# Kernel optimization log

Hardware: AMD Instinct MI355X
Metric: run time of the kernel (lower is better)

The kernel has to match this reference:

```python
import jax, jax.numpy as jnp
import numpy as np

B, T, C, H = 2, 2048, 1024, 16
D = C // H  # head_dim = 64


def setup_inputs() -> dict:
    key = jax.random.key(0)
    ks = jax.random.split(key, 12)
    s = 1.0 / np.sqrt(C)
    inp = {
        "q": jax.random.normal(ks[0], (B, T, C), jnp.float32),
        "k": jax.random.normal(ks[1], (B, T, C), jnp.float32),
        "v": jax.random.normal(ks[2], (B, T, C), jnp.float32),
        "mask": jnp.tril(jnp.ones((T, T), jnp.int32)),  # causal mask; 0 = masked
        "Wq": jax.random.normal(ks[3], (C, C), jnp.float32) * s,
        "bq": jax.random.normal(ks[4], (C,), jnp.float32) * s,
        "Wk": jax.random.normal(ks[5], (C, C), jnp.float32) * s,
        "bk": jax.random.normal(ks[6], (C,), jnp.float32) * s,
        "Wv": jax.random.normal(ks[7], (C, C), jnp.float32) * s,
        "bv": jax.random.normal(ks[8], (C,), jnp.float32) * s,
        "Wo": jax.random.normal(ks[9], (C, C), jnp.float32) * s,
        "bo": jax.random.normal(ks[10], (C,), jnp.float32) * s,
    }
    return inp


def reference(q, k, v, mask, Wq, bq, Wk, bk, Wv, bv, Wo, bo):
    # Linear projections (torch Linear: x @ W.T + b)
    qh = (q @ Wq.T + bq).reshape(B, T, H, D).transpose(0, 2, 1, 3)  # [B,H,T,D]
    kh = (k @ Wk.T + bk).reshape(B, -1, H, D).transpose(0, 2, 1, 3)
    vh = (v @ Wv.T + bv).reshape(B, -1, H, D).transpose(0, 2, 1, 3)
    scores = jnp.einsum("bhtd,bhsd->bhts", qh, kh) / jnp.sqrt(jnp.float32(D))
    scores = jnp.where(mask[None, None, :, :] == 0, -jnp.inf, scores)
    attn = jax.nn.softmax(scores, axis=-1)
    out = jnp.einsum("bhts,bhsd->bhtd", attn, vh)  # [B,H,T,D]
    out = out.transpose(0, 2, 1, 3).reshape(B, T, C)
    return out @ Wo.T + bo
```

## Files before the change

### kernel.cpp

```cpp
#include <hip/hip_runtime.h>
#include <hip/hip_bf16.h>

#define BB 2
#define TT 2048
#define CC 1024
#define HH 16
#define DD 64
#define MM (BB * TT)

typedef __bf16 bf16;
typedef __bf16 bf16x4 __attribute__((ext_vector_type(4)));
typedef __bf16 bf16x8 __attribute__((ext_vector_type(8)));
typedef float f32x4 __attribute__((ext_vector_type(4)));

__device__ __forceinline__ void gload16(const bf16* g, bf16* l) {
    __builtin_amdgcn_global_load_lds(
        (__attribute__((address_space(1))) void*)g,
        (__attribute__((address_space(3))) void*)l, 16, 0, 0);
}

__global__ __launch_bounds__(256) void to_bf16(
    const float* __restrict__ q, const float* __restrict__ k,
    const float* __restrict__ v,
    const float* __restrict__ wq, const float* __restrict__ wk,
    const float* __restrict__ wv, const float* __restrict__ wo,
    bf16* __restrict__ xq, bf16* __restrict__ xk, bf16* __restrict__ xv,
    bf16* __restrict__ owq, bf16* __restrict__ owk, bf16* __restrict__ owv,
    bf16* __restrict__ owo)
{
    const unsigned XE = 1u << 22;
    const unsigned WE = 1u << 20;
    const unsigned NC = (3u * XE + 4u * WE) >> 3;
    for (unsigned c = blockIdx.x * blockDim.x + threadIdx.x; c < NC;
         c += gridDim.x * blockDim.x) {
        const unsigned e = c << 3;
        const float* src; bf16* dst; unsigned off;
        if (e < 3u * XE) {
            const unsigned t = e >> 22; off = e & (XE - 1u);
            src = (t == 0) ? q : (t == 1) ? k : v;
            dst = (t == 0) ? xq : (t == 1) ? xk : xv;
        } else {
            const unsigned e2 = e - 3u * XE;
            const unsigned t = e2 >> 20; off = e2 & (WE - 1u);
            src = (t == 0) ? wq : (t == 1) ? wk : (t == 2) ? wv : wo;
            dst = (t == 0) ? owq : (t == 1) ? owk : (t == 2) ? owv : owo;
        }
        const f32x4 a = *reinterpret_cast<const f32x4*>(src + off);
        const f32x4 b = *reinterpret_cast<const f32x4*>(src + off + 4);
        bf16x8 r;
#pragma unroll
        for (int j = 0; j < 4; ++j) { r[j] = (bf16)a[j]; r[j + 4] = (bf16)b[j]; }
        *reinterpret_cast<bf16x8*>(dst + off) = r;
    }
}

template <typename TOUT, int HEAD_LAYOUT>
__device__ __forceinline__ void gemm_tile_body(
    const bf16* __restrict__ X, const bf16* __restrict__ W,
    const float* __restrict__ bias, TOUT* __restrict__ out,
    bf16* lA, bf16* lB, int vmode)
{
    const int tid  = threadIdx.x;
    const int lane = tid & 63;
    const int quad = lane >> 4;
    const int lm   = lane & 15;
    const int wave = tid >> 6;
    const int m0 = blockIdx.x << 7;
    const int n0 = blockIdx.y << 7;
    const int wrow = (wave >> 1) << 6;
    const int wcol = (wave & 1) << 6;

    const int c0 = tid, c1 = tid + 256;
    const bf16* gA0 = X + (size_t)(m0 + (c0 >> 2)) * CC + (c0 & 3) * 8;
    const bf16* gA1 = X + (size_t)(m0 + (c1 >> 2)) * CC + (c1 & 3) * 8;
    const bf16* gB0 = W + (size_t)(n0 + (c0 >> 2)) * CC + (c0 & 3) * 8;
    const bf16* gB1 = W + (size_t)(n0 + (c1 >> 2)) * CC + (c1 & 3) * 8;
    bf16* lAw0 = lA + wave * 512;
    bf16* lAw1 = lA + 2048 + wave * 512;
    bf16* lBw0 = lB + wave * 512;
    bf16* lBw1 = lB + 2048 + wave * 512;

    f32x4 acc[4][4];
#pragma unroll
    for (int i = 0; i < 4; ++i)
#pragma unroll
        for (int j = 0; j < 4; ++j) acc[i][j] = (f32x4){0.f, 0.f, 0.f, 0.f};

    for (int kk = 0; kk < CC; kk += 32) {
        __syncthreads();
        gload16(gA0 + kk, lAw0);
        gload16(gA1 + kk, lAw1);
        gload16(gB0 + kk, lBw0);
        gload16(gB1 + kk, lBw1);
        __syncthreads();

        bf16x8 af[4], bf_[4];
#pragma unroll
        for (int i = 0; i < 4; ++i)
            af[i] = *reinterpret_cast<const bf16x8*>(
                lA + (wrow + i * 16 + lm) * 32 + quad * 8);
#pragma unroll
        for (int j = 0; j < 4; ++j)
            bf_[j] = *reinterpret_cast<const bf16x8*>(
                lB + (wcol + j * 16 + lm) * 32 + quad * 8);
#pragma unroll
        for (int i = 0; i < 4; ++i)
#pragma unroll
            for (int j = 0; j < 4; ++j)
                acc[i][j] = __builtin_amdgcn_mfma_f32_16x16x32_bf16(
                    af[i], bf_[j], acc[i][j], 0, 0, 0);
    }

#pragma unroll
    for (int j = 0; j < 4; ++j) {
        const int col = n0 + wcol + j * 16 + lm;
        const float bv = bias[col];
        if (vmode) {
            const int h = col / DD, d = col % DD;
#pragma unroll
            for (int i = 0; i < 4; ++i) {
                const int m = m0 + wrow + i * 16 + quad * 4;
                const int b_ = m / TT, t = m % TT;
                bf16x4 o;
#pragma unroll
                for (int r = 0; r < 4; ++r) o[r] = (bf16)(acc[i][j][r] + bv);
                *reinterpret_cast<bf16x4*>(
                    (bf16*)out + (((size_t)(b_ * HH + h)) * DD + d) * TT + t) = o;
            }
        } else {
#pragma unroll
            for (int i = 0; i < 4; ++i)
#pragma unroll
                for (int r = 0; r < 4; ++r) {
                    const int m = m0 + wrow + i * 16 + quad * 4 + r;
                    const float v = acc[i][j][r] + bv;
                    if (HEAD_LAYOUT) {
                        const int b_ = m / TT, t = m % TT;
                        const int h = col / DD, d = col % DD;
                        out[(((size_t)(b_ * HH + h)) * TT + t) * DD + d] = (TOUT)v;
                    } else {
                        out[(size_t)m * CC + col] = (TOUT)v;
                    }
                }
        }
    }
}

__global__ __launch_bounds__(256) void gemm_qkv(
    const bf16* __restrict__ x0, const bf16* __restrict__ x1,
    const bf16* __restrict__ x2,
    const bf16* __restrict__ w0, const bf16* __restrict__ w1,
    const bf16* __restrict__ w2,
    const float* __restrict__ b0, const float* __restrict__ b1,
    const float* __restrict__ b2,
    bf16* __restrict__ o0, bf16* __restrict__ o1, bf16* __restrict__ o2)
{
    __shared__ __align__(16) bf16 lA[128 * 32];
    __shared__ __align__(16) bf16 lB[128 * 32];
    const int z = blockIdx.z;
    const bf16* X = (z == 0) ? x0 : (z == 1) ? x1 : x2;
    const bf16* W = (z == 0) ? w0 : (z == 1) ? w1 : w2;
    const float* bias = (z == 0) ? b0 : (z == 1) ? b1 : b2;
    bf16* out = (z == 0) ? o0 : (z == 1) ? o1 : o2;
    gemm_tile_body<bf16, 1>(X, W, bias, out, lA, lB, (z == 2) ? 1 : 0);
}

__global__ __launch_bounds__(256) void gemm_oproj(
    const bf16* __restrict__ X, const bf16* __restrict__ W,
    const float* __restrict__ bias, float* __restrict__ out)
{
    __shared__ __align__(16) bf16 lA[128 * 32];
    __shared__ __align__(16) bf16 lB[128 * 32];
    gemm_tile_body<float, 0>(X, W, bias, out, lA, lB, 0);
}

__global__ __launch_bounds__(256) void attn_fused(
    const bf16* __restrict__ Qh, const bf16* __restrict__ Kh,
    const bf16* __restrict__ Vt, bf16* __restrict__ attn_out)
{
    __shared__ __align__(16) bf16 ldsK[64 * 72];
    __shared__ __align__(16) bf16 ldsV[16 * 64 * 4];

    const int tid  = threadIdx.x;
    const int lane = tid & 63;
    const int wave = tid >> 6;
    const int xp = blockIdx.x;
    const int bh = blockIdx.y;
    const int b_ = bh >> 4, h = bh & 15;
    const size_t baseQK = (size_t)bh * TT * DD;
    const size_t baseVT = (size_t)bh * DD * TT;
    const int lm   = lane & 15;
    const int quad = lane >> 4;
    const int koff = quad * 8;

    const int kKey = tid >> 3, kDc = tid & 7;
    const int vD   = tid >> 2, vSc = tid & 3;

    for (int pass = 0; pass < 2; ++pass) {
        const int qb = pass == 0 ? (TT / 64 - 1 - xp) : xp;
        const int q0 = qb * 64 + wave * 16;
        const int q_lane = q0 + lm;

        const bf16* qp = Qh + baseQK + (size_t)q_lane * DD + koff;
        bf16x8 qr0 = *reinterpret_cast<const bf16x8*>(qp);
        bf16x8 qr1 = *reinterpret_cast<const bf16x8*>(qp + 32);
        bf16x8 qf0, qf1;
#pragma unroll
        for (int j = 0; j < 8; ++j) {
            qf0[j] = (bf16)((float)qr0[j] * 0.125f);
            qf1[j] = (bf16)((float)qr1[j] * 0.125f);
        }

        f32x4 Oacc[4];
#pragma unroll
        for (int dt = 0; dt < 4; ++dt) Oacc[dt] = (f32x4){0.f, 0.f, 0.f, 0.f};
        float m_run = -1e30f, l_run = 0.f;

        for (int kb = 0; kb <= qb; ++kb) {
            const int s0 = kb * 64;

            __syncthreads();
#pragma unroll
            for (int it = 0; it < 2; ++it) {
                const int key = kKey + it * 32;
                bf16x8 kv = *reinterpret_cast<const bf16x8*>(
                    Kh + baseQK + (size_t)(s0 + key) * DD + kDc * 8);
                *reinterpret_cast<bf16x8*>(&ldsK[key * 72 + kDc * 8]) = kv;
            }
#pragma unroll
            for (int it = 0; it < 2; ++it) {
                const int sc = vSc + it * 4;
                bf16x8 vv = *reinterpret_cast<const bf16x8*>(
                    Vt + baseVT + (size_t)vD * TT + s0 + sc * 8);
                bf16x4 lo, hi;
#pragma unroll
                for (int j = 0; j < 4; ++j) { lo[j] = vv[j]; hi[j] = vv[4 + j]; }
                *reinterpret_cast<bf16x4*>(&ldsV[((2 * sc) * 64 + vD) * 4]) = lo;
                *reinterpret_cast<bf16x4*>(&ldsV[((2 * sc + 1) * 64 + vD) * 4]) = hi;
            }
            __syncthreads();

            float sv[4][4];
#pragma unroll
            for (int st = 0; st < 4; ++st) {
                const bf16* kp = &ldsK[(st * 16 + lm) * 72 + koff];
                bf16x8 k0 = *reinterpret_cast<const bf16x8*>(kp);
                bf16x8 k1 = *reinterpret_cast<const bf16x8*>(kp + 32);
                f32x4 s = {0.f, 0.f, 0.f, 0.f};
                s = __builtin_amdgcn_mfma_f32_16x16x32_bf16(k0, qf0, s, 0, 0, 0);
                s = __builtin_amdgcn_mfma_f32_16x16x32_bf16(k1, qf1, s, 0, 0, 0);
#pragma unroll
                for (int r = 0; r < 4; ++r) sv[st][r] = s[r];
            }
            if (kb == qb) {
#pragma unroll
                for (int st = 0; st < 4; ++st) {
                    const int kbase = s0 + st * 16 + quad * 4;
#pragma unroll
                    for (int r = 0; r < 4; ++r)
                        if (kbase + r > q_lane) sv[st][r] = -1e30f;
                }
            }

            float mx = sv[0][0];
#pragma unroll
            for (int st = 0; st < 4; ++st)
#pragma unroll
                for (int r = 0; r < 4; ++r) mx = fmaxf(mx, sv[st][r]);
            mx = fmaxf(mx, __shfl_xor(mx, 16));
            mx = fmaxf(mx, __shfl_xor(mx, 32));
            if (__any(mx > m_run)) {
                const float mn = fmaxf(m_run, mx);
                const float alpha = __expf(m_run - mn);
                m_run = mn;
                l_run *= alpha;
#pragma unroll
                for (int dt = 0; dt < 4; ++dt) Oacc[dt] *= alpha;
            }
            float srow = 0.f;
#pragma unroll
            for (int st = 0; st < 4; ++st)
#pragma unroll
                for (int r = 0; r < 4; ++r) {
                    const float p = __expf(sv[st][r] - m_run);
                    sv[st][r] = p;
                    srow += p;
                }
            srow += __shfl_xor(srow, 16);
            srow += __shfl_xor(srow, 32);
            l_run += srow;

            bf16x8 pf[2];
#pragma unroll
            for (int c = 0; c < 2; ++c)
#pragma unroll
                for (int j = 0; j < 4; ++j) {
                    pf[c][j]     = (bf16)sv[2 * c][j];
                    pf[c][4 + j] = (bf16)sv[2 * c + 1][j];
                }

#pragma unroll
            for (int dt = 0; dt < 4; ++dt) {
                const int d = dt * 16 + lm;
#pragma unroll
                for (int c = 0; c < 2; ++c) {
                    bf16x4 v0 = *reinterpret_cast<const bf16x4*>(
                        &ldsV[((c * 8 + quad) * 64 + d) * 4]);
                    bf16x4 v1 = *reinterpret_cast<const bf16x4*>(
                        &ldsV[((c * 8 + 4 + quad) * 64 + d) * 4]);
                    bf16x8 vf;
#pragma unroll
                    for (int j = 0; j < 4; ++j) { vf[j] = v0[j]; vf[4 + j] = v1[j]; }
                    Oacc[dt] = __builtin_amdgcn_mfma_f32_16x16x32_bf16(
                        vf, pf[c], Oacc[dt], 0, 0, 0);
                }
            }
        }

        const float inv_l = 1.0f / l_run;
        bf16* dst = attn_out + ((size_t)(b_ * TT + q_lane)) * CC + h * DD;
#pragma unroll
        for (int dt = 0; dt < 4; ++dt) {
            bf16x4 o;
#pragma unroll
            for (int r = 0; r < 4; ++r) o[r] = (bf16)(Oacc[dt][r] * inv_l);
            *reinterpret_cast<bf16x4*>(dst + dt * 16 + quad * 4) = o;
        }
    }
}

extern "C" void kernel_launch(void* const* d_in, const int* in_sizes, int n_in,
                              void* d_out, int out_size, void* d_ws,
                              size_t ws_size, hipStream_t stream)
{
    const float* q  = (const float*)d_in[0];
    const float* k  = (const float*)d_in[1];
    const float* v  = (const float*)d_in[2];
    const float* Wq = (const float*)d_in[4];
    const float* bq = (const float*)d_in[5];
    const float* Wk = (const float*)d_in[6];
    const float* bk = (const float*)d_in[7];
    const float* Wv = (const float*)d_in[8];
    const float* bv = (const float*)d_in[9];
    const float* Wo = (const float*)d_in[10];
    const float* bo = (const float*)d_in[11];
    float* out = (float*)d_out;

    bf16* Qh   = (bf16*)d_ws;
    bf16* Kh   = Qh + (size_t)MM * CC;
    bf16* Vt   = Kh + (size_t)MM * CC;
    bf16* attn = Vt + (size_t)MM * CC;
    bf16* Xq   = attn + (size_t)MM * CC;
    bf16* Xk   = Xq + (size_t)MM * CC;
    bf16* Xv   = Xk + (size_t)MM * CC;
    bf16* Wqb  = Xv + (size_t)MM * CC;
    bf16* Wkb  = Wqb + (size_t)CC * CC;
    bf16* Wvb  = Wkb + (size_t)CC * CC;
    bf16* Wob  = Wvb + (size_t)CC * CC;

    const dim3 blk(256);
    to_bf16<<<dim3(2048), blk, 0, stream>>>(
        q, k, v, Wq, Wk, Wv, Wo, Xq, Xk, Xv, Wqb, Wkb, Wvb, Wob);
    gemm_qkv<<<dim3(MM / 128, CC / 128, 3), blk, 0, stream>>>(
        Xq, Xk, Xv, Wqb, Wkb, Wvb, bq, bk, bv, Qh, Kh, Vt);
    attn_fused<<<dim3(TT / 128, BB * HH), blk, 0, stream>>>(Qh, Kh, Vt, attn);
    gemm_oproj<<<dim3(MM / 128, CC / 128), blk, 0, stream>>>(
        attn, Wob, bo, out);
}
```

Before: 240.3 us.

## Double-buffer K/V tiles in attention with register prefetch and MFMA priority

The attention kernel now keeps two LDS buffers for the K and V tiles. It prefetches the next key block's K/V into registers while the current block is being computed, which removes one barrier per iteration and overlaps global-load latency with MFMA work. It also wraps the MFMA sections in s_setprio to favour matrix issue. The cost is doubled LDS use and extra registers, which may lower occupancy.

After: 234.7 us. 2.3% less time.

```diff
diff --git a/kernel.cpp b/kernel.cpp
--- a/kernel.cpp
+++ b/kernel.cpp
@@ -178,8 +178,8 @@
     const bf16* __restrict__ Qh, const bf16* __restrict__ Kh,
     const bf16* __restrict__ Vt, bf16* __restrict__ attn_out)
 {
-    __shared__ __align__(16) bf16 ldsK[64 * 72];
-    __shared__ __align__(16) bf16 ldsV[16 * 64 * 4];
+    __shared__ __align__(16) bf16 ldsK[2][64 * 72];
+    __shared__ __align__(16) bf16 ldsV[2][16 * 64 * 4];
 
     const int tid  = threadIdx.x;
     const int lane = tid & 63;
@@ -216,34 +216,55 @@
         for (int dt = 0; dt < 4; ++dt) Oacc[dt] = (f32x4){0.f, 0.f, 0.f, 0.f};
         float m_run = -1e30f, l_run = 0.f;
 
+        bf16x8 kreg[2], vreg[2];
+#pragma unroll
+        for (int it = 0; it < 2; ++it) {
+            kreg[it] = *reinterpret_cast<const bf16x8*>(
+                Kh + baseQK + (size_t)(kKey + it * 32) * DD + kDc * 8);
+            vreg[it] = *reinterpret_cast<const bf16x8*>(
+                Vt + baseVT + (size_t)vD * TT + (vSc + it * 4) * 8);
+        }
+        __syncthreads();
+
         for (int kb = 0; kb <= qb; ++kb) {
-            const int s0 = kb * 64;
-
-            __syncthreads();
+            const int cur = kb & 1;
+
 #pragma unroll
             for (int it = 0; it < 2; ++it) {
                 const int key = kKey + it * 32;
-                bf16x8 kv = *reinterpret_cast<const bf16x8*>(
-                    Kh + baseQK + (size_t)(s0 + key) * DD + kDc * 8);
-                *reinterpret_cast<bf16x8*>(&ldsK[key * 72 + kDc * 8]) = kv;
-            }
-#pragma unroll
-            for (int it = 0; it < 2; ++it) {
+                *reinterpret_cast<bf16x8*>(
+                    &ldsK[cur][key * 72 + kDc * 8]) = kreg[it];
                 const int sc = vSc + it * 4;
-                bf16x8 vv = *reinterpret_cast<const bf16x8*>(
-                    Vt + baseVT + (size_t)vD * TT + s0 + sc * 8);
                 bf16x4 lo, hi;
 #pragma unroll
-                for (int j = 0; j < 4; ++j) { lo[j] = vv[j]; hi[j] = vv[4 + j]; }
-                *reinterpret_cast<bf16x4*>(&ldsV[((2 * sc) * 64 + vD) * 4]) = lo;
-                *reinterpret_cast<bf16x4*>(&ldsV[((2 * sc + 1) * 64 + vD) * 4]) = hi;
+                for (int j = 0; j < 4; ++j) {
+                    lo[j] = vreg[it][j]; hi[j] = vreg[it][4 + j];
+                }
+                *reinterpret_cast<bf16x4*>(
+                    &ldsV[cur][((2 * sc) * 64 + vD) * 4]) = lo;
+                *reinterpret_cast<bf16x4*>(
+                    &ldsV[cur][((2 * sc + 1) * 64 + vD) * 4]) = hi;
             }
             __syncthreads();
 
+            if (kb < qb) {
+                const int s0n = (kb + 1) * 64;
+#pragma unroll
+                for (int it = 0; it < 2; ++it) {
+                    kreg[it] = *reinterpret_cast<const bf16x8*>(
+                        Kh + baseQK + (size_t)(s0n + kKey + it * 32) * DD
+                        + kDc * 8);
+                    vreg[it] = *reinterpret_cast<const bf16x8*>(
+                        Vt + baseVT + (size_t)vD * TT + s0n
+                        + (vSc + it * 4) * 8);
+                }
+            }
+
             float sv[4][4];
+            __builtin_amdgcn_s_setprio(1);
 #pragma unroll
             for (int st = 0; st < 4; ++st) {
-                const bf16* kp = &ldsK[(st * 16 + lm) * 72 + koff];
+                const bf16* kp = &ldsK[cur][(st * 16 + lm) * 72 + koff];
                 bf16x8 k0 = *reinterpret_cast<const bf16x8*>(kp);
                 bf16x8 k1 = *reinterpret_cast<const bf16x8*>(kp + 32);
                 f32x4 s = {0.f, 0.f, 0.f, 0.f};
@@ -252,7 +273,10 @@
 #pragma unroll
                 for (int r = 0; r < 4; ++r) sv[st][r] = s[r];
             }
+            __builtin_amdgcn_s_setprio(0);
+
             if (kb == qb) {
+                const int s0 = kb * 64;
 #pragma unroll
                 for (int st = 0; st < 4; ++st) {
                     const int kbase = s0 + st * 16 + quad * 4;
@@ -299,15 +323,16 @@
                     pf[c][4 + j] = (bf16)sv[2 * c + 1][j];
                 }
 
+            __builtin_amdgcn_s_setprio(1);
 #pragma unroll
             for (int dt = 0; dt < 4; ++dt) {
                 const int d = dt * 16 + lm;
 #pragma unroll
                 for (int c = 0; c < 2; ++c) {
                     bf16x4 v0 = *reinterpret_cast<const bf16x4*>(
-                        &ldsV[((c * 8 + quad) * 64 + d) * 4]);
+                        &ldsV[cur][((c * 8 + quad) * 64 + d) * 4]);
                     bf16x4 v1 = *reinterpret_cast<const bf16x4*>(
-                        &ldsV[((c * 8 + 4 + quad) * 64 + d) * 4]);
+                        &ldsV[cur][((c * 8 + 4 + quad) * 64 + d) * 4]);
                     bf16x8 vf;
 #pragma unroll
                     for (int j = 0; j < 4; ++j) { vf[j] = v0[j]; vf[4 + j] = v1[j]; }
@@ -315,6 +340,7 @@
                         vf, pf[c], Oacc[dt], 0, 0, 0);
                 }
             }
+            __builtin_amdgcn_s_setprio(0);
         }
 
         const float inv_l = 1.0f / l_run;
```
